# Kernel optimization log

Measured on AMD Instinct MI355X. Metric: run time of the kernel, lower is better.

Reference implementation:

```python
import jax, jax.numpy as jnp
import numpy as np

B, N, M, D = 2, 2048, 32, 128
H, DH = 8, 16
DI = H * DH            # dim_inner = 128
S = 5                  # 1 + max_degree + max_degree, max_degree = 2
DMLP = 256             # int(2.0 * dim_inner)


def _ln(x, g):  # LayerNorm(bias=False)
    mu = x.mean(-1, keepdims=True)
    var = ((x - mu) ** 2).mean(-1, keepdims=True)
    return (x - mu) / jnp.sqrt(var + 1e-5) * g


def _softclamp(t, v=50.0):
    return jnp.tanh(t / v) * v


def _gather(a, idx):  # a: [b, n, ...], idx: [b, i, j] -> [b, i, j, ...]
    return jax.vmap(lambda t, ix: jnp.take(t, ix, axis=0))(a, idx)


def setup_inputs():
    key = jax.random.key(0)
    ks = jax.random.split(key, 24)
    w = lambda k, i, o: jax.random.normal(k, (i, o), jnp.float32) / np.sqrt(i)
    return {
        'h': jax.random.normal(ks[0], (B, N, D), jnp.float32),
        't_ij': jax.random.normal(ks[1], (B, N, M, D), jnp.float32),
        'r_ij_1': jax.random.normal(ks[2], (B, N, M, 3), jnp.float32),
        'r_ij_2': jax.random.normal(ks[3], (B, N, M, 5), jnp.float32),
        'x_1': jax.random.normal(ks[4], (B, N, D, 3), jnp.float32),
        'x_2': jax.random.normal(ks[5], (B, N, D, 5), jnp.float32),
        'g_hi': jnp.ones((D,), jnp.float32),
        'g_hj': jnp.ones((D,), jnp.float32),
        'Wq': w(ks[6], D, DI),
        'Wk': w(ks[7], D, DI),
        'Wv1': w(ks[8], D, DMLP), 'bv1': jnp.zeros((DMLP,), jnp.float32),
        'Wv2': w(ks[9], DMLP, S * DI), 'bv2': jnp.zeros((S * DI,), jnp.float32),
        'Wp1': w(ks[10], D, DMLP), 'bp1': jnp.zeros((DMLP,), jnp.float32),
        'Wp2': w(ks[11], DMLP, S * DI), 'bp2': jnp.zeros((S * DI,), jnp.float32),
        'Wek': w(ks[12], D, S * DI),
        'Wev': w(ks[13], D, S * DI),
        'Wg': w(ks[14], D, H * S), 'bg': jnp.zeros((H * S,), jnp.float32),
        'Wc': w(ks[15], DI, D),
        'neighbor_indices': jax.random.randint(ks[16], (B, N, M), 0, N),
        'neighbor_mask': jnp.ones((B, N, M), bool),
    }


def reference(h, t_ij, r_ij_1, r_ij_2, x_1, x_2, g_hi, g_hj, Wq, Wk, Wv1, bv1,
              Wv2, bv2, Wp1, bp1, Wp2, bp2, Wek, Wev, Wg, bg, Wc,
              neighbor_indices, neighbor_mask):
    b, n, m = neighbor_indices.shape
    hi = _ln(h, g_hi)
    hj = _ln(h, g_hj)
    q = (hi @ Wq).reshape(b, n, H, DH).transpose(0, 2, 1, 3)               # b h i dh
    k = hj @ Wk                                                            # b n (h dh)
    v = jax.nn.silu(hj @ Wv1 + bv1) @ Wv2 + bv2                            # b n (s h dh)
    pav = jax.nn.silu(hj @ Wp1 + bp1) @ Wp2 + bp2                          # post-attn h values
    ek = jax.nn.silu(t_ij @ Wek)                                           # b i j (s h dh)
    ev = t_ij @ Wev
    # neighbor gathers over the node axis
    k_g = _gather(k, neighbor_indices)                                     # b i j (h dh)
    v_g = _gather(v, neighbor_indices)                                     # b i j (s h dh)
    pav_g = _gather(pav, neighbor_indices)
    heads4 = lambda t: t.reshape(b, n, m, H, DH).transpose(0, 3, 1, 2, 4)          # b h i j dh
    heads5 = lambda t: t.reshape(b, n, m, S, H, DH).transpose(0, 4, 1, 2, 3, 5)    # b h i j s dh
    keys = heads4(k_g)[..., None, :] * heads5(ek)                          # edge-fused keys
    sim = _softclamp(jnp.einsum('bhid,bhijsd->bhijs', q, keys))
    sim = jnp.where(neighbor_mask[:, None, :, :, None], sim, -jnp.finfo(sim.dtype).max)
    attn = jax.nn.softmax(sim, axis=-2)                                    # softmax over neighbors j
    sea = attn[..., None] * heads5(v_g) + heads5(ev) * heads5(pav_g)       # b h i j s dh
    gates = jax.nn.sigmoid(hi @ Wg + bg).reshape(b, n, H, S)               # layout (h s)
    sea = sea * gates.transpose(0, 2, 1, 3)[:, :, :, None, :, None]        # b h i 1 s 1
    out = sea.transpose(0, 2, 3, 4, 1, 5).reshape(b, n, m, S, DI) @ Wc     # b i j s d
    h_res = out[..., 0, :].sum(axis=2)                                     # sum over neighbors
    x_res = []
    for li, (r_l, x_l) in enumerate(((r_ij_1, x_1), (r_ij_2, x_2))):
        r_part = jnp.einsum('bijm,bijd->bidm', r_l, out[..., 1 + li, :])
        xg = _gather(x_l, neighbor_indices)                                # b i j d ml
        x_res.append(r_part + jnp.einsum('bijdm,bijd->bidm', xg, out[..., 3 + li, :]))
    return (h_res, x_res[0], x_res[1])
```

## Files before the change

kernel.cpp:

```cpp
#include <hip/hip_runtime.h>
#include <hip/hip_bf16.h>
#include <cstdint>


typedef __bf16 bf16x8 __attribute__((ext_vector_type(8)));
typedef float  f32x4  __attribute__((ext_vector_type(4)));
typedef unsigned short u16;
typedef unsigned int   u32;

__device__ __forceinline__ float sigm_(float x){ return 1.f/(1.f+__expf(-x)); }
__device__ __forceinline__ float silu_(float x){ return x/(1.f+__expf(-x)); }
__device__ __forceinline__ u16 f2b(float f){
    union{float f; u32 u;} x; x.f = f;
    u32 r = x.u + 0x7FFFu + ((x.u>>16)&1u);
    return (u16)(r>>16);
}
__device__ __forceinline__ float b2f(u16 b){
    union{u32 u; float f;} x; x.u = ((u32)b)<<16; return x.f;
}
union VecU { uint4 u; bf16x8 v; u16 s[8]; };
union Vec4 { uint2 u; u16 s[4]; };
__device__ __forceinline__ bf16x8 ld8(const u16* p){ VecU x; x.u = *(const uint4*)p; return x.v; }

__global__ __launch_bounds__(256) void prep_kernel(
    const float* __restrict__ Wek, const float* __restrict__ Wev,
    const float* __restrict__ Wc,
    const float* __restrict__ x1, const float* __restrict__ x2,
    u16* __restrict__ wekT, u16* __restrict__ wevT, u16* __restrict__ wcT,
    float* __restrict__ xT1, float* __restrict__ xT2, int do_xt)
{
    const int idx = blockIdx.x*256 + threadIdx.x;
    if (idx < 81920) {
        const int n = idx >> 7, k = idx & 127;
        wekT[idx] = f2b(Wek[k*640 + n]);
        wevT[idx] = f2b(Wev[k*640 + n]);
    }
    if (idx < 16384) {
        const int d = idx >> 7, c = idx & 127;
        wcT[idx] = f2b(Wc[c*128 + d]);
    }
    if (do_xt) {
        if (idx < 4096*384) {
            const int node = idx/384, rem = idx%384, m = rem>>7, d = rem&127;
            xT1[idx] = x1[((size_t)node*128 + d)*3 + m];
        }
        if (idx < 4096*640) {
            const int node = idx/640, rem = idx%640, m = rem>>7, d = rem&127;
            xT2[idx] = x2[((size_t)node*128 + d)*5 + m];
        }
    }
}

__global__ __launch_bounds__(256) void node_kernel(
    const float* __restrict__ h,
    const float* __restrict__ g_hi, const float* __restrict__ g_hj,
    const float* __restrict__ Wq, const float* __restrict__ Wk,
    const float* __restrict__ Wv1, const float* __restrict__ bv1,
    const float* __restrict__ Wv2, const float* __restrict__ bv2,
    const float* __restrict__ Wp1, const float* __restrict__ bp1,
    const float* __restrict__ Wp2, const float* __restrict__ bp2,
    const float* __restrict__ Wg, const float* __restrict__ bg,
    float* __restrict__ qws, float* __restrict__ kws,
    float* __restrict__ vws, float* __restrict__ pavws, float* __restrict__ gws)
{
    const int tid  = threadIdx.x;
    const int base = blockIdx.x * 8;
    __shared__ __align__(16) float hi_s[8][128];
    __shared__ __align__(16) float hj_s[8][128];
    __shared__ __align__(16) float u_s[8][256];

    {
        const int wv = tid >> 6, lane = tid & 63;
        for (int r = wv; r < 8; r += 4) {
            const int node = base + r;
            float a  = h[node*128 + lane];
            float b2 = h[node*128 + 64 + lane];
            float s = a + b2;
            #pragma unroll
            for (int off = 32; off > 0; off >>= 1) s += __shfl_down(s, off);
            s = __shfl(s, 0);
            const float mu = s * (1.f/128.f);
            const float da = a - mu, db = b2 - mu;
            float v = da*da + db*db;
            #pragma unroll
            for (int off = 32; off > 0; off >>= 1) v += __shfl_down(v, off);
            v = __shfl(v, 0);
            const float rstd = rsqrtf(v*(1.f/128.f) + 1e-5f);
            hi_s[r][lane]    = da*rstd*g_hi[lane];
            hi_s[r][64+lane] = db*rstd*g_hi[64+lane];
            hj_s[r][lane]    = da*rstd*g_hj[lane];
            hj_s[r][64+lane] = db*rstd*g_hj[64+lane];
        }
    }
    __syncthreads();

    {
        const int o  = tid & 127;
        const int r0 = (tid >> 7) * 4;
        float aq[4], ak[4];
        #pragma unroll
        for (int r=0;r<4;r++){ aq[r]=0.f; ak[r]=0.f; }
        for (int c0=0;c0<128;c0+=4) {
            float wq0=Wq[(c0+0)*128+o], wq1=Wq[(c0+1)*128+o], wq2=Wq[(c0+2)*128+o], wq3=Wq[(c0+3)*128+o];
            float wk0=Wk[(c0+0)*128+o], wk1=Wk[(c0+1)*128+o], wk2=Wk[(c0+2)*128+o], wk3=Wk[(c0+3)*128+o];
            #pragma unroll
            for (int r=0;r<4;r++) {
                float4 hi4 = *(const float4*)(&hi_s[r0+r][c0]);
                float4 hj4 = *(const float4*)(&hj_s[r0+r][c0]);
                aq[r] += hi4.x*wq0; aq[r] += hi4.y*wq1; aq[r] += hi4.z*wq2; aq[r] += hi4.w*wq3;
                ak[r] += hj4.x*wk0; ak[r] += hj4.y*wk1; ak[r] += hj4.z*wk2; ak[r] += hj4.w*wk3;
            }
        }
        #pragma unroll
        for (int r=0;r<4;r++) {
            qws[(size_t)(base+r0+r)*128 + o] = aq[r];
            kws[(size_t)(base+r0+r)*128 + o] = ak[r];
        }
    }

    {
        const int o = tid;
        float acc[8];
        const float bias = bv1[o];
        #pragma unroll
        for (int r=0;r<8;r++) acc[r]=bias;
        for (int c0=0;c0<128;c0+=4) {
            float w0=Wv1[(c0+0)*256+o], w1=Wv1[(c0+1)*256+o], w2=Wv1[(c0+2)*256+o], w3=Wv1[(c0+3)*256+o];
            #pragma unroll
            for (int r=0;r<8;r++) {
                float4 u4 = *(const float4*)(&hj_s[r][c0]);
                acc[r] += u4.x*w0; acc[r] += u4.y*w1; acc[r] += u4.z*w2; acc[r] += u4.w*w3;
            }
        }
        #pragma unroll
        for (int r=0;r<8;r++) u_s[r][o] = silu_(acc[r]);
    }
    __syncthreads();

    for (int o=tid; o<640; o+=256) {
        float acc[8];
        const float bias = bv2[o];
        #pragma unroll
        for (int r=0;r<8;r++) acc[r]=bias;
        for (int c0=0;c0<256;c0+=4) {
            float w0=Wv2[(c0+0)*640+o], w1=Wv2[(c0+1)*640+o], w2=Wv2[(c0+2)*640+o], w3=Wv2[(c0+3)*640+o];
            #pragma unroll
            for (int r=0;r<8;r++) {
                float4 u4 = *(const float4*)(&u_s[r][c0]);
                acc[r] += u4.x*w0; acc[r] += u4.y*w1; acc[r] += u4.z*w2; acc[r] += u4.w*w3;
            }
        }
        #pragma unroll
        for (int r=0;r<8;r++) vws[(size_t)(base+r)*640 + o] = acc[r];
    }
    __syncthreads();

    {
        const int o = tid;
        float acc[8];
        const float bias = bp1[o];
        #pragma unroll
        for (int r=0;r<8;r++) acc[r]=bias;
        for (int c0=0;c0<128;c0+=4) {
            float w0=Wp1[(c0+0)*256+o], w1=Wp1[(c0+1)*256+o], w2=Wp1[(c0+2)*256+o], w3=Wp1[(c0+3)*256+o];
            #pragma unroll
            for (int r=0;r<8;r++) {
                float4 u4 = *(const float4*)(&hj_s[r][c0]);
                acc[r] += u4.x*w0; acc[r] += u4.y*w1; acc[r] += u4.z*w2; acc[r] += u4.w*w3;
            }
        }
        #pragma unroll
        for (int r=0;r<8;r++) u_s[r][o] = silu_(acc[r]);
    }
    __syncthreads();

    for (int o=tid; o<640; o+=256) {
        float acc[8];
        const float bias = bp2[o];
        #pragma unroll
        for (int r=0;r<8;r++) acc[r]=bias;
        for (int c0=0;c0<256;c0+=4) {
            float w0=Wp2[(c0+0)*640+o], w1=Wp2[(c0+1)*640+o], w2=Wp2[(c0+2)*640+o], w3=Wp2[(c0+3)*640+o];
            #pragma unroll
            for (int r=0;r<8;r++) {
                float4 u4 = *(const float4*)(&u_s[r][c0]);
                acc[r] += u4.x*w0; acc[r] += u4.y*w1; acc[r] += u4.z*w2; acc[r] += u4.w*w3;
            }
        }
        #pragma unroll
        for (int r=0;r<8;r++) pavws[(size_t)(base+r)*640 + o] = acc[r];
    }

    for (int idx=tid; idx<8*40; idx+=256) {
        const int r = idx/40, hs = idx%40;
        float s = bg[hs];
        for (int c=0;c<128;c++) s += hi_s[r][c]*Wg[c*40+hs];
        gws[(size_t)(base+r)*40 + hs] = sigm_(s);
    }
}

template<bool XT>
__global__ __launch_bounds__(256,3) void edge_kernel(
    const float* __restrict__ t_ij,
    const float* __restrict__ r1, const float* __restrict__ r2,
    const float* __restrict__ x1, const float* __restrict__ x2,
    const float* __restrict__ xT1, const float* __restrict__ xT2,
    const u16* __restrict__ wekT, const u16* __restrict__ wevT,
    const u16* __restrict__ wcT,
    const int* __restrict__ nidx,
    const float* __restrict__ qws, const float* __restrict__ kws,
    const float* __restrict__ vws, const float* __restrict__ pavws,
    const float* __restrict__ gws,
    float* __restrict__ out)
{
    const int node = blockIdx.x;
    const int bN   = (node >> 11) << 11;
    const int tid  = threadIdx.x;
    const int lane = tid & 63, w = tid >> 6;
    const int ll   = lane & 15, lh = lane >> 4;

    __shared__ __align__(16) u16   tj_s[32*128];
    __shared__ __align__(16) u16   chunk_s[80*128];
    __shared__ float sim_s[32][40];
    __shared__ __align__(16) float q_s[128];
    __shared__ float g_s[40];
    __shared__ int   jn_s[32];

    if (tid < 32) jn_s[tid] = nidx[node*32 + tid];
    else if (tid >= 64 && tid < 192) q_s[tid-64] = qws[(size_t)node*128 + (tid-64)];
    else if (tid >= 192 && tid < 232) g_s[tid-192] = gws[(size_t)node*40 + (tid-192)];
    __syncthreads();

    bf16x8 wcf[2][4];
    #pragma unroll
    for (int dlt=0;dlt<2;dlt++)
        #pragma unroll
        for (int ks=0;ks<4;ks++)
            wcf[dlt][ks] = ld8(wcT + (size_t)((w*2+dlt)*16 + ll)*128 + ks*32 + lh*8);

    float kq[16];
    {
        const int j = tid >> 3, c0 = (tid & 7) * 16;
        const float* tp = t_ij + (size_t)node*4096 + j*128 + c0;
        float4 t0 = *(const float4*)(tp+0);
        float4 t1 = *(const float4*)(tp+4);
        float4 t2 = *(const float4*)(tp+8);
        float4 t3 = *(const float4*)(tp+12);
        VecU p0, p1;
        p0.s[0]=f2b(t0.x); p0.s[1]=f2b(t0.y); p0.s[2]=f2b(t0.z); p0.s[3]=f2b(t0.w);
        p0.s[4]=f2b(t1.x); p0.s[5]=f2b(t1.y); p0.s[6]=f2b(t1.z); p0.s[7]=f2b(t1.w);
        p1.s[0]=f2b(t2.x); p1.s[1]=f2b(t2.y); p1.s[2]=f2b(t2.z); p1.s[3]=f2b(t2.w);
        p1.s[4]=f2b(t3.x); p1.s[5]=f2b(t3.y); p1.s[6]=f2b(t3.z); p1.s[7]=f2b(t3.w);
        const int el = (j*128 + c0) ^ ((j&7)<<3);
        *(uint4*)(tj_s + el)       = p0.u;
        *(uint4*)(tj_s + (el ^ 8)) = p1.u;

        const float* kp = kws + ((size_t)(bN + jn_s[j]))*128 + c0;
        #pragma unroll
        for (int i=0;i<16;i+=4) {
            float4 kv = *(const float4*)(kp+i);
            float4 qv = *(const float4*)(&q_s[c0+i]);
            kq[i+0] = qv.x*kv.x; kq[i+1] = qv.y*kv.y;
            kq[i+2] = qv.z*kv.z; kq[i+3] = qv.w*kv.w;
        }
    }
    __syncthreads();

    for (int jh=0; jh<2; jh++) {
        bf16x8 tfr[4];
        #pragma unroll
        for (int ks=0;ks<4;ks++) {
            const int j = jh*16 + ll;
            tfr[ks] = ld8(tj_s + ((j*128 + ks*32 + lh*8) ^ ((j&7)<<3)));
        }
        #pragma unroll 2
        for (int t=0;t<10;t++) {
            const int nt = w + 4*t;
            const u16* wp = wekT + (size_t)(nt*16 + ll)*128 + lh*8;
            __builtin_amdgcn_s_setprio(1);
            f32x4 aA = {0.f,0.f,0.f,0.f}, aB = {0.f,0.f,0.f,0.f};
            aA = __builtin_amdgcn_mfma_f32_16x16x32_bf16(ld8(wp +  0), tfr[0], aA, 0,0,0);
            aB = __builtin_amdgcn_mfma_f32_16x16x32_bf16(ld8(wp + 32), tfr[1], aB, 0,0,0);
            aA = __builtin_amdgcn_mfma_f32_16x16x32_bf16(ld8(wp + 64), tfr[2], aA, 0,0,0);
            aB = __builtin_amdgcn_mfma_f32_16x16x32_bf16(ld8(wp + 96), tfr[3], aB, 0,0,0);
            __builtin_amdgcn_s_setprio(0);
            f32x4 acc = aA + aB;
            const int ss = nt >> 3, c0 = (nt&7)*16 + lh*4;
            const int r  = ss*16 + ll;
            Vec4 pk;
            #pragma unroll
            for (int reg=0;reg<4;reg++) pk.s[reg] = f2b(silu_(acc[reg]));
            *(uint2*)(chunk_s + ((r*128 + c0) ^ ((r&7)<<3))) = pk.u;
        }
        __syncthreads();

        if ((tid >> 7) == jh) {
            const int jj = (tid >> 3) & 15, hh = tid & 7;
            #pragma unroll
            for (int ss=0; ss<5; ss++) {
                const int r = ss*16 + jj;
                const int el = (r*128 + hh*16) ^ ((r&7)<<3);
                VecU e0, e1;
                e0.u = *(const uint4*)(chunk_s + el);
                e1.u = *(const uint4*)(chunk_s + (el^8));
                float s = 0.f;
                #pragma unroll
                for (int i=0;i<8;i++) s += kq[i]   * b2f(e0.s[i]);
                #pragma unroll
                for (int i=0;i<8;i++) s += kq[8+i] * b2f(e1.s[i]);
                sim_s[jh*16 + jj][hh*5 + ss] = 50.f * tanhf(s*0.02f);
            }
        }
        __syncthreads();
    }

    if (tid < 40) {
        float mx = -1e30f;
        #pragma unroll
        for (int j=0;j<32;j++) mx = fmaxf(mx, sim_s[j][tid]);
        float sum = 0.f;
        #pragma unroll
        for (int j=0;j<32;j++) sum += __expf(sim_s[j][tid]-mx);
        const float inv = 1.f/sum;
        #pragma unroll
        for (int j=0;j<32;j++) sim_s[j][tid] = __expf(sim_s[j][tid]-mx)*inv;
    }
    __syncthreads();

    float accH[2] = {0,0};
    float aR1[3][2], aX1[3][2], aR2[5][2], aX2[5][2];
    #pragma unroll
    for (int m=0;m<3;m++){ aR1[m][0]=aR1[m][1]=0.f; aX1[m][0]=aX1[m][1]=0.f; }
    #pragma unroll
    for (int m=0;m<5;m++){ aR2[m][0]=aR2[m][1]=0.f; aX2[m][0]=aX2[m][1]=0.f; }

    for (int jh=0; jh<2; jh++) {
        bf16x8 tfr[4];
        #pragma unroll
        for (int ks=0;ks<4;ks++) {
            const int j = jh*16 + ll;
            tfr[ks] = ld8(tj_s + ((j*128 + ks*32 + lh*8) ^ ((j&7)<<3)));
        }
        const int edge = jh*16 + ll;
        const int nj   = jn_s[edge];
        const float* vrow = vws   + (size_t)(bN + nj)*640;
        const float* prow = pavws + (size_t)(bN + nj)*640;

        float4 v4c = *(const float4*)(vrow + (w*16 + lh*4));
        float4 pvc = *(const float4*)(prow + (w*16 + lh*4));
        #pragma unroll 2
        for (int t=0;t<10;t++) {
            const int nt = w + 4*t;
            const float4 v4 = v4c, pv = pvc;
            if (t < 9) {
                const int o0n = (nt+4)*16 + lh*4;
                v4c = *(const float4*)(vrow + o0n);
                pvc = *(const float4*)(prow + o0n);
            }
            const u16* wp = wevT + (size_t)(nt*16 + ll)*128 + lh*8;
            __builtin_amdgcn_s_setprio(1);
            f32x4 aA = {0.f,0.f,0.f,0.f}, aB = {0.f,0.f,0.f,0.f};
            aA = __builtin_amdgcn_mfma_f32_16x16x32_bf16(ld8(wp +  0), tfr[0], aA, 0,0,0);
            aB = __builtin_amdgcn_mfma_f32_16x16x32_bf16(ld8(wp + 32), tfr[1], aB, 0,0,0);
            aA = __builtin_amdgcn_mfma_f32_16x16x32_bf16(ld8(wp + 64), tfr[2], aA, 0,0,0);
            aB = __builtin_amdgcn_mfma_f32_16x16x32_bf16(ld8(wp + 96), tfr[3], aB, 0,0,0);
            __builtin_amdgcn_s_setprio(0);
            f32x4 acc = aA + aB;
            const int ss = nt >> 3, hsu = (nt&7)*5 + ss;
            const int c0 = (nt&7)*16 + lh*4;
            const float gate = g_s[hsu];
            const float attn = sim_s[edge][hsu];
            Vec4 w4;
            w4.s[0] = f2b((attn*v4.x + acc[0]*pv.x)*gate);
            w4.s[1] = f2b((attn*v4.y + acc[1]*pv.y)*gate);
            w4.s[2] = f2b((attn*v4.z + acc[2]*pv.z)*gate);
            w4.s[3] = f2b((attn*v4.w + acc[3]*pv.w)*gate);
            const int r = ss*16 + ll;
            *(uint2*)(chunk_s + ((r*128 + c0) ^ ((r&7)<<3))) = w4.u;
        }
        __syncthreads();

        #pragma unroll 1
        for (int mt=0; mt<5; ++mt) {
            bf16x8 afr[4];
            #pragma unroll
            for (int ks=0;ks<4;ks++) {
                const int r = mt*16 + ll;
                afr[ks] = ld8(chunk_s + ((r*128 + ks*32 + lh*8) ^ ((r&7)<<3)));
            }
            #pragma unroll
            for (int dlt=0; dlt<2; ++dlt) {
                __builtin_amdgcn_s_setprio(1);
                f32x4 dA = {0.f,0.f,0.f,0.f}, dB = {0.f,0.f,0.f,0.f};
                dA = __builtin_amdgcn_mfma_f32_16x16x32_bf16(afr[0], wcf[dlt][0], dA, 0,0,0);
                dB = __builtin_amdgcn_mfma_f32_16x16x32_bf16(afr[1], wcf[dlt][1], dB, 0,0,0);
                dA = __builtin_amdgcn_mfma_f32_16x16x32_bf16(afr[2], wcf[dlt][2], dA, 0,0,0);
                dB = __builtin_amdgcn_mfma_f32_16x16x32_bf16(afr[3], wcf[dlt][3], dB, 0,0,0);
                __builtin_amdgcn_s_setprio(0);
                f32x4 dacc = dA + dB;
                const int d = (w*2+dlt)*16 + ll;
                if (mt == 0) {
                    accH[dlt] += dacc[0]+dacc[1]+dacc[2]+dacc[3];
                } else if (mt == 1) {
                    #pragma unroll
                    for (int reg=0;reg<4;reg++) {
                        const int j = jh*16 + lh*4 + reg;
                        const float* rp = r1 + ((size_t)node*32 + j)*3;
                        const float p = dacc[reg];
                        #pragma unroll
                        for (int m=0;m<3;m++) aR1[m][dlt] += rp[m]*p;
                    }
                } else if (mt == 2) {
                    #pragma unroll
                    for (int reg=0;reg<4;reg++) {
                        const int j = jh*16 + lh*4 + reg;
                        const float* rp = r2 + ((size_t)node*32 + j)*5;
                        const float p = dacc[reg];
                        #pragma unroll
                        for (int m=0;m<5;m++) aR2[m][dlt] += rp[m]*p;
                    }
                } else if (mt == 3) {
                    #pragma unroll
                    for (int reg=0;reg<4;reg++) {
                        const int j = jh*16 + lh*4 + reg;
                        const int njg = jn_s[j];
                        const float p = dacc[reg];
                        if (XT) {
                            const float* xp = xT1 + ((size_t)(bN + njg)*3)*128 + d;
                            #pragma unroll
                            for (int m=0;m<3;m++) aX1[m][dlt] += xp[m*128]*p;
                        } else {
                            const float* xp = x1 + ((size_t)(bN + njg)*128 + d)*3;
                            #pragma unroll
                            for (int m=0;m<3;m++) aX1[m][dlt] += xp[m]*p;
                        }
                    }
                } else {
                    #pragma unroll
                    for (int reg=0;reg<4;reg++) {
                        const int j = jh*16 + lh*4 + reg;
                        const int njg = jn_s[j];
                        const float p = dacc[reg];
                        if (XT) {
                            const float* xp = xT2 + ((size_t)(bN + njg)*5)*128 + d;
                            #pragma unroll
                            for (int m=0;m<5;m++) aX2[m][dlt] += xp[m*128]*p;
                        } else {
                            const float* xp = x2 + ((size_t)(bN + njg)*128 + d)*5;
                            #pragma unroll
                            for (int m=0;m<5;m++) aX2[m][dlt] += xp[m]*p;
                        }
                    }
                }
            }
        }
        __syncthreads();
    }

    #define RED2(x) { x += __shfl_xor(x,16); x += __shfl_xor(x,32); }
    #pragma unroll
    for (int dlt=0; dlt<2; ++dlt) {
        RED2(accH[dlt]);
        #pragma unroll
        for (int m=0;m<3;m++){ RED2(aR1[m][dlt]); RED2(aX1[m][dlt]); }
        #pragma unroll
        for (int m=0;m<5;m++){ RED2(aR2[m][dlt]); RED2(aX2[m][dlt]); }
    }
    if (lh == 0) {
        #pragma unroll
        for (int dlt=0; dlt<2; ++dlt) {
            const int d = (w*2+dlt)*16 + ll;
            out[(size_t)node*128 + d] = accH[dlt];
            float* o1 = out + 524288 + ((size_t)node*128 + d)*3;
            #pragma unroll
            for (int m=0;m<3;m++) o1[m] = aR1[m][dlt] + aX1[m][dlt];
            float* o2 = out + 2097152 + ((size_t)node*128 + d)*5;
            #pragma unroll
            for (int m=0;m<5;m++) o2[m] = aR2[m][dlt] + aX2[m][dlt];
        }
    }
}

extern "C" void kernel_launch(void* const* d_in, const int* in_sizes, int n_in,
                              void* d_out, int out_size, void* d_ws, size_t ws_size,
                              hipStream_t stream)
{
    const float* h    = (const float*)d_in[0];
    const float* t_ij = (const float*)d_in[1];
    const float* r1   = (const float*)d_in[2];
    const float* r2   = (const float*)d_in[3];
    const float* x1   = (const float*)d_in[4];
    const float* x2   = (const float*)d_in[5];
    const float* g_hi = (const float*)d_in[6];
    const float* g_hj = (const float*)d_in[7];
    const float* Wq   = (const float*)d_in[8];
    const float* Wk   = (const float*)d_in[9];
    const float* Wv1  = (const float*)d_in[10];
    const float* bv1  = (const float*)d_in[11];
    const float* Wv2  = (const float*)d_in[12];
    const float* bv2  = (const float*)d_in[13];
    const float* Wp1  = (const float*)d_in[14];
    const float* bp1  = (const float*)d_in[15];
    const float* Wp2  = (const float*)d_in[16];
    const float* bp2  = (const float*)d_in[17];
    const float* Wek  = (const float*)d_in[18];
    const float* Wev  = (const float*)d_in[19];
    const float* Wg   = (const float*)d_in[20];
    const float* bg   = (const float*)d_in[21];
    const float* Wc   = (const float*)d_in[22];
    const int*   nidx = (const int*)d_in[23];

    char* ws = (char*)d_ws;
    float* qws   = (float*)ws;  ws += (size_t)4096*128*4;
    float* kws   = (float*)ws;  ws += (size_t)4096*128*4;
    float* gws   = (float*)ws;  ws += (size_t)4096*40*4;
    float* vws   = (float*)ws;  ws += (size_t)4096*640*4;
    float* pavws = (float*)ws;  ws += (size_t)4096*640*4;
    u16*   wekT  = (u16*)ws;    ws += (size_t)81920*2;
    u16*   wevT  = (u16*)ws;    ws += (size_t)81920*2;
    u16*   wcT   = (u16*)ws;    ws += (size_t)16384*2;
    float* xT1   = (float*)ws;  ws += (size_t)4096*384*4;
    float* xT2   = (float*)ws;  ws += (size_t)4096*640*4;
    const size_t need_xt = (size_t)(ws - (char*)d_ws);
    const int use_xt = (ws_size >= need_xt) ? 1 : 0;

    hipLaunchKernelGGL(prep_kernel, dim3(use_xt ? 10240 : 320), dim3(256), 0, stream,
        Wek, Wev, Wc, x1, x2, wekT, wevT, wcT, xT1, xT2, use_xt);

    hipLaunchKernelGGL(node_kernel, dim3(512), dim3(256), 0, stream,
        h, g_hi, g_hj, Wq, Wk, Wv1, bv1, Wv2, bv2, Wp1, bp1, Wp2, bp2, Wg, bg,
        qws, kws, vws, pavws, gws);

    if (use_xt) {
        hipLaunchKernelGGL(edge_kernel<true>, dim3(4096), dim3(256), 0, stream,
            t_ij, r1, r2, x1, x2, xT1, xT2, wekT, wevT, wcT, nidx,
            qws, kws, vws, pavws, gws, (float*)d_out);
    } else {
        hipLaunchKernelGGL(edge_kernel<false>, dim3(4096), dim3(256), 0, stream,
            t_ij, r1, r2, x1, x2, xT1, xT2, wekT, wevT, wcT, nidx,
            qws, kws, vws, pavws, gws, (float*)d_out);
    }
}
```

Before: 577.3 us.

## Split edge kernel into two 256-thread groups processing neighbor halves concurrently

The edge kernel goes from 256 to 512 threads per block. Each group of 256 threads handles one half of the 32 neighbors in parallel, where before a single group looped over the halves one after another. Each group gets its own chunk buffer in shared memory, and the groups' partial reductions are combined through shared memory before the final write. This removes the serial loop over halves and several block barriers, but it doubles chunk shared memory, keeps the Wc fragments in registers in both groups, and adds a cross-group reduction step. The launch bounds change to (512,4), which may limit registers per thread.

```diff
diff --git a/kernel.cpp b/kernel.cpp
--- a/kernel.cpp
+++ b/kernel.cpp
@@ -200,7 +200,7 @@
 }
 
 template<bool XT>
-__global__ __launch_bounds__(256,3) void edge_kernel(
+__global__ __launch_bounds__(512,4) void edge_kernel(
     const float* __restrict__ t_ij,
     const float* __restrict__ r1, const float* __restrict__ r2,
     const float* __restrict__ x1, const float* __restrict__ x2,
@@ -216,16 +216,20 @@
     const int node = blockIdx.x;
     const int bN   = (node >> 11) << 11;
     const int tid  = threadIdx.x;
-    const int lane = tid & 63, w = tid >> 6;
+    const int grp  = tid >> 8;
+    const int ltid = tid & 255;
+    const int lane = ltid & 63, w = ltid >> 6;
     const int ll   = lane & 15, lh = lane >> 4;
 
     __shared__ __align__(16) u16   tj_s[32*128];
-    __shared__ __align__(16) u16   chunk_s[80*128];
+    __shared__ __align__(16) u16   chunk_s[2][80*128];
     __shared__ float sim_s[32][40];
     __shared__ __align__(16) float q_s[128];
     __shared__ float g_s[40];
     __shared__ int   jn_s[32];
 
+    u16* chunk = chunk_s[grp];
+
     if (tid < 32) jn_s[tid] = nidx[node*32 + tid];
     else if (tid >= 64 && tid < 192) q_s[tid-64] = qws[(size_t)node*128 + (tid-64)];
     else if (tid >= 192 && tid < 232) g_s[tid-192] = gws[(size_t)node*40 + (tid-192)];
@@ -239,8 +243,8 @@
             wcf[dlt][ks] = ld8(wcT + (size_t)((w*2+dlt)*16 + ll)*128 + ks*32 + lh*8);
 
     float kq[16];
-    {
-        const int j = tid >> 3, c0 = (tid & 7) * 16;
+    if (ltid < 128) {
+        const int j = grp*16 + (ltid >> 3), c0 = (ltid & 7) * 16;
         const float* tp = t_ij + (size_t)node*4096 + j*128 + c0;
         float4 t0 = *(const float4*)(tp+0);
         float4 t1 = *(const float4*)(tp+4);
@@ -266,53 +270,51 @@
     }
     __syncthreads();
 
-    for (int jh=0; jh<2; jh++) {
-        bf16x8 tfr[4];
-        #pragma unroll
-        for (int ks=0;ks<4;ks++) {
-            const int j = jh*16 + ll;
-            tfr[ks] = ld8(tj_s + ((j*128 + ks*32 + lh*8) ^ ((j&7)<<3)));
-        }
-        #pragma unroll 2
-        for (int t=0;t<10;t++) {
-            const int nt = w + 4*t;
-            const u16* wp = wekT + (size_t)(nt*16 + ll)*128 + lh*8;
-            __builtin_amdgcn_s_setprio(1);
-            f32x4 aA = {0.f,0.f,0.f,0.f}, aB = {0.f,0.f,0.f,0.f};
-            aA = __builtin_amdgcn_mfma_f32_16x16x32_bf16(ld8(wp +  0), tfr[0], aA, 0,0,0);
-            aB = __builtin_amdgcn_mfma_f32_16x16x32_bf16(ld8(wp + 32), tfr[1], aB, 0,0,0);
-            aA = __builtin_amdgcn_mfma_f32_16x16x32_bf16(ld8(wp + 64), tfr[2], aA, 0,0,0);
-            aB = __builtin_amdgcn_mfma_f32_16x16x32_bf16(ld8(wp + 96), tfr[3], aB, 0,0,0);
-            __builtin_amdgcn_s_setprio(0);
-            f32x4 acc = aA + aB;
-            const int ss = nt >> 3, c0 = (nt&7)*16 + lh*4;
-            const int r  = ss*16 + ll;
-            Vec4 pk;
-            #pragma unroll
-            for (int reg=0;reg<4;reg++) pk.s[reg] = f2b(silu_(acc[reg]));
-            *(uint2*)(chunk_s + ((r*128 + c0) ^ ((r&7)<<3))) = pk.u;
-        }
-        __syncthreads();
-
-        if ((tid >> 7) == jh) {
-            const int jj = (tid >> 3) & 15, hh = tid & 7;
-            #pragma unroll
-            for (int ss=0; ss<5; ss++) {
-                const int r = ss*16 + jj;
-                const int el = (r*128 + hh*16) ^ ((r&7)<<3);
-                VecU e0, e1;
-                e0.u = *(const uint4*)(chunk_s + el);
-                e1.u = *(const uint4*)(chunk_s + (el^8));
-                float s = 0.f;
-                #pragma unroll
-                for (int i=0;i<8;i++) s += kq[i]   * b2f(e0.s[i]);
-                #pragma unroll
-                for (int i=0;i<8;i++) s += kq[8+i] * b2f(e1.s[i]);
-                sim_s[jh*16 + jj][hh*5 + ss] = 50.f * tanhf(s*0.02f);
-            }
-        }
-        __syncthreads();
-    }
+    bf16x8 tfr[4];
+    #pragma unroll
+    for (int ks=0;ks<4;ks++) {
+        const int j = grp*16 + ll;
+        tfr[ks] = ld8(tj_s + ((j*128 + ks*32 + lh*8) ^ ((j&7)<<3)));
+    }
+    #pragma unroll 2
+    for (int t=0;t<10;t++) {
+        const int nt = w + 4*t;
+        const u16* wp = wekT + (size_t)(nt*16 + ll)*128 + lh*8;
+        __builtin_amdgcn_s_setprio(1);
+        f32x4 aA = {0.f,0.f,0.f,0.f}, aB = {0.f,0.f,0.f,0.f};
+        aA = __builtin_amdgcn_mfma_f32_16x16x32_bf16(ld8(wp +  0), tfr[0], aA, 0,0,0);
+        aB = __builtin_amdgcn_mfma_f32_16x16x32_bf16(ld8(wp + 32), tfr[1], aB, 0,0,0);
+        aA = __builtin_amdgcn_mfma_f32_16x16x32_bf16(ld8(wp + 64), tfr[2], aA, 0,0,0);
+        aB = __builtin_amdgcn_mfma_f32_16x16x32_bf16(ld8(wp + 96), tfr[3], aB, 0,0,0);
+        __builtin_amdgcn_s_setprio(0);
+        f32x4 acc = aA + aB;
+        const int ss = nt >> 3, c0 = (nt&7)*16 + lh*4;
+        const int r  = ss*16 + ll;
+        Vec4 pk;
+        #pragma unroll
+        for (int reg=0;reg<4;reg++) pk.s[reg] = f2b(silu_(acc[reg]));
+        *(uint2*)(chunk + ((r*128 + c0) ^ ((r&7)<<3))) = pk.u;
+    }
+    __syncthreads();
+
+    if (ltid < 128) {
+        const int jj = ltid >> 3, hh = ltid & 7;
+        #pragma unroll
+        for (int ss=0; ss<5; ss++) {
+            const int r = ss*16 + jj;
+            const int el = (r*128 + hh*16) ^ ((r&7)<<3);
+            VecU e0, e1;
+            e0.u = *(const uint4*)(chunk + el);
+            e1.u = *(const uint4*)(chunk + (el^8));
+            float s = 0.f;
+            #pragma unroll
+            for (int i=0;i<8;i++) s += kq[i]   * b2f(e0.s[i]);
+            #pragma unroll
+            for (int i=0;i<8;i++) s += kq[8+i] * b2f(e1.s[i]);
+            sim_s[grp*16 + jj][hh*5 + ss] = 50.f * tanhf(s*0.02f);
+        }
+    }
+    __syncthreads();
 
     if (tid < 40) {
         float mx = -1e30f;
@@ -334,14 +336,8 @@
     #pragma unroll
     for (int m=0;m<5;m++){ aR2[m][0]=aR2[m][1]=0.f; aX2[m][0]=aX2[m][1]=0.f; }
 
-    for (int jh=0; jh<2; jh++) {
-        bf16x8 tfr[4];
-        #pragma unroll
-        for (int ks=0;ks<4;ks++) {
-            const int j = jh*16 + ll;
-            tfr[ks] = ld8(tj_s + ((j*128 + ks*32 + lh*8) ^ ((j&7)<<3)));
-        }
-        const int edge = jh*16 + ll;
+    {
+        const int edge = grp*16 + ll;
         const int nj   = jn_s[edge];
         const float* vrow = vws   + (size_t)(bN + nj)*640;
         const float* prow = pavws + (size_t)(bN + nj)*640;
@@ -376,85 +372,84 @@
             w4.s[2] = f2b((attn*v4.z + acc[2]*pv.z)*gate);
             w4.s[3] = f2b((attn*v4.w + acc[3]*pv.w)*gate);
             const int r = ss*16 + ll;
-            *(uint2*)(chunk_s + ((r*128 + c0) ^ ((r&7)<<3))) = w4.u;
-        }
-        __syncthreads();
-
-        #pragma unroll 1
-        for (int mt=0; mt<5; ++mt) {
-            bf16x8 afr[4];
-            #pragma unroll
-            for (int ks=0;ks<4;ks++) {
-                const int r = mt*16 + ll;
-                afr[ks] = ld8(chunk_s + ((r*128 + ks*32 + lh*8) ^ ((r&7)<<3)));
-            }
-            #pragma unroll
-            for (int dlt=0; dlt<2; ++dlt) {
-                __builtin_amdgcn_s_setprio(1);
-                f32x4 dA = {0.f,0.f,0.f,0.f}, dB = {0.f,0.f,0.f,0.f};
-                dA = __builtin_amdgcn_mfma_f32_16x16x32_bf16(afr[0], wcf[dlt][0], dA, 0,0,0);
-                dB = __builtin_amdgcn_mfma_f32_16x16x32_bf16(afr[1], wcf[dlt][1], dB, 0,0,0);
-                dA = __builtin_amdgcn_mfma_f32_16x16x32_bf16(afr[2], wcf[dlt][2], dA, 0,0,0);
-                dB = __builtin_amdgcn_mfma_f32_16x16x32_bf16(afr[3], wcf[dlt][3], dB, 0,0,0);
-                __builtin_amdgcn_s_setprio(0);
-                f32x4 dacc = dA + dB;
-                const int d = (w*2+dlt)*16 + ll;
-                if (mt == 0) {
-                    accH[dlt] += dacc[0]+dacc[1]+dacc[2]+dacc[3];
-                } else if (mt == 1) {
+            *(uint2*)(chunk + ((r*128 + c0) ^ ((r&7)<<3))) = w4.u;
+        }
+    }
+    __syncthreads();
+
+    #pragma unroll 1
+    for (int mt=0; mt<5; ++mt) {
+        bf16x8 afr[4];
+        #pragma unroll
+        for (int ks=0;ks<4;ks++) {
+            const int r = mt*16 + ll;
+            afr[ks] = ld8(chunk + ((r*128 + ks*32 + lh*8) ^ ((r&7)<<3)));
+        }
+        #pragma unroll
+        for (int dlt=0; dlt<2; ++dlt) {
+            __builtin_amdgcn_s_setprio(1);
+            f32x4 dA = {0.f,0.f,0.f,0.f}, dB = {0.f,0.f,0.f,0.f};
+            dA = __builtin_amdgcn_mfma_f32_16x16x32_bf16(afr[0], wcf[dlt][0], dA, 0,0,0);
+            dB = __builtin_amdgcn_mfma_f32_16x16x32_bf16(afr[1], wcf[dlt][1], dB, 0,0,0);
+            dA = __builtin_amdgcn_mfma_f32_16x16x32_bf16(afr[2], wcf[dlt][2], dA, 0,0,0);
+            dB = __builtin_amdgcn_mfma_f32_16x16x32_bf16(afr[3], wcf[dlt][3], dB, 0,0,0);
+            __builtin_amdgcn_s_setprio(0);
+            f32x4 dacc = dA + dB;
+            const int d = (w*2+dlt)*16 + ll;
+            if (mt == 0) {
+                accH[dlt] += dacc[0]+dacc[1]+dacc[2]+dacc[3];
+            } else if (mt == 1) {
+                #pragma unroll
+                for (int reg=0;reg<4;reg++) {
+                    const int j = grp*16 + lh*4 + reg;
+                    const float* rp = r1 + ((size_t)node*32 + j)*3;
+                    const float p = dacc[reg];
                     #pragma unroll
-                    for (int reg=0;reg<4;reg++) {
-                        const int j = jh*16 + lh*4 + reg;
-                        const float* rp = r1 + ((size_t)node*32 + j)*3;
-                        const float p = dacc[reg];
+                    for (int m=0;m<3;m++) aR1[m][dlt] += rp[m]*p;
+                }
+            } else if (mt == 2) {
+                #pragma unroll
+                for (int reg=0;reg<4;reg++) {
+                    const int j = grp*16 + lh*4 + reg;
+                    const float* rp = r2 + ((size_t)node*32 + j)*5;
+                    const float p = dacc[reg];
+                    #pragma unroll
+                    for (int m=0;m<5;m++) aR2[m][dlt] += rp[m]*p;
+                }
+            } else if (mt == 3) {
+                #pragma unroll
+                for (int reg=0;reg<4;reg++) {
+                    const int j = grp*16 + lh*4 + reg;
+                    const int njg = jn_s[j];
+                    const float p = dacc[reg];
+                    if (XT) {
+                        const float* xp = xT1 + ((size_t)(bN + njg)*3)*128 + d;
                         #pragma unroll
-                        for (int m=0;m<3;m++) aR1[m][dlt] += rp[m]*p;
-                    }
-                } else if (mt == 2) {
-                    #pragma unroll
-                    for (int reg=0;reg<4;reg++) {
-                        const int j = jh*16 + lh*4 + reg;
-                        const float* rp = r2 + ((size_t)node*32 + j)*5;
-                        const float p = dacc[reg];
+                        for (int m=0;m<3;m++) aX1[m][dlt] += xp[m*128]*p;
+                    } else {
+                        const float* xp = x1 + ((size_t)(bN + njg)*128 + d)*3;
                         #pragma unroll
-                        for (int m=0;m<5;m++) aR2[m][dlt] += rp[m]*p;
-                    }
-                } else if (mt == 3) {
-                    #pragma unroll
-                    for (int reg=0;reg<4;reg++) {
-                        const int j = jh*16 + lh*4 + reg;
-                        const int njg = jn_s[j];
-                        const float p = dacc[reg];
-                        if (XT) {
-                            const float* xp = xT1 + ((size_t)(bN + njg)*3)*128 + d;
-                            #pragma unroll
-                            for (int m=0;m<3;m++) aX1[m][dlt] += xp[m*128]*p;
-                        } else {
-                            const float* xp = x1 + ((size_t)(bN + njg)*128 + d)*3;
-                            #pragma unroll
-                            for (int m=0;m<3;m++) aX1[m][dlt] += xp[m]*p;
-                        }
-                    }
-                } else {
-                    #pragma unroll
-                    for (int reg=0;reg<4;reg++) {
-                        const int j = jh*16 + lh*4 + reg;
-                        const int njg = jn_s[j];
-                        const float p = dacc[reg];
-                        if (XT) {
-                            const float* xp = xT2 + ((size_t)(bN + njg)*5)*128 + d;
-                            #pragma unroll
-                            for (int m=0;m<5;m++) aX2[m][dlt] += xp[m*128]*p;
-                        } else {
-                            const float* xp = x2 + ((size_t)(bN + njg)*128 + d)*5;
-                            #pragma unroll
-                            for (int m=0;m<5;m++) aX2[m][dlt] += xp[m]*p;
-                        }
+                        for (int m=0;m<3;m++) aX1[m][dlt] += xp[m]*p;
                     }
                 }
-            }
-        }
-        __syncthreads();
+            } else {
+                #pragma unroll
+                for (int reg=0;reg<4;reg++) {
+                    const int j = grp*16 + lh*4 + reg;
+                    const int njg = jn_s[j];
+                    const float p = dacc[reg];
+                    if (XT) {
+                        const float* xp = xT2 + ((size_t)(bN + njg)*5)*128 + d;
+                        #pragma unroll
+                        for (int m=0;m<5;m++) aX2[m][dlt] += xp[m*128]*p;
+                    } else {
+                        const float* xp = x2 + ((size_t)(bN + njg)*128 + d)*5;
+                        #pragma unroll
+                        for (int m=0;m<5;m++) aX2[m][dlt] += xp[m]*p;
+                    }
+                }
+            }
+        }
     }
 
     #define RED2(x) { x += __shfl_xor(x,16); x += __shfl_xor(x,32); }
@@ -466,17 +461,34 @@
         #pragma unroll
         for (int m=0;m<5;m++){ RED2(aR2[m][dlt]); RED2(aX2[m][dlt]); }
     }
-    if (lh == 0) {
+    __syncthreads();
+
+    float* xch = (float*)chunk_s[0];
+    if (grp == 1 && lh == 0) {
         #pragma unroll
         for (int dlt=0; dlt<2; ++dlt) {
             const int d = (w*2+dlt)*16 + ll;
-            out[(size_t)node*128 + d] = accH[dlt];
+            float* p = xch + d*17;
+            p[0] = accH[dlt];
+            #pragma unroll
+            for (int m=0;m<3;m++){ p[1+m] = aR1[m][dlt]; p[4+m] = aX1[m][dlt]; }
+            #pragma unroll
+            for (int m=0;m<5;m++){ p[7+m] = aR2[m][dlt]; p[12+m] = aX2[m][dlt]; }
+        }
+    }
+    __syncthreads();
+    if (grp == 0 && lh == 0) {
+        #pragma unroll
+        for (int dlt=0; dlt<2; ++dlt) {
+            const int d = (w*2+dlt)*16 + ll;
+            const float* p = xch + d*17;
+            out[(size_t)node*128 + d] = accH[dlt] + p[0];
             float* o1 = out + 524288 + ((size_t)node*128 + d)*3;
             #pragma unroll
-            for (int m=0;m<3;m++) o1[m] = aR1[m][dlt] + aX1[m][dlt];
+            for (int m=0;m<3;m++) o1[m] = (aR1[m][dlt] + p[1+m]) + (aX1[m][dlt] + p[4+m]);
             float* o2 = out + 2097152 + ((size_t)node*128 + d)*5;
             #pragma unroll
-            for (int m=0;m<5;m++) o2[m] = aR2[m][dlt] + aX2[m][dlt];
+            for (int m=0;m<5;m++) o2[m] = (aR2[m][dlt] + p[7+m]) + (aX2[m][dlt] + p[12+m]);
         }
     }
 }
@@ -532,11 +544,11 @@
         qws, kws, vws, pavws, gws);
 
     if (use_xt) {
-        hipLaunchKernelGGL(edge_kernel<true>, dim3(4096), dim3(256), 0, stream,
+        hipLaunchKernelGGL(edge_kernel<true>, dim3(4096), dim3(512), 0, stream,
             t_ij, r1, r2, x1, x2, xT1, xT2, wekT, wevT, wcT, nidx,
             qws, kws, vws, pavws, gws, (float*)d_out);
     } else {
-        hipLaunchKernelGGL(edge_kernel<false>, dim3(4096), dim3(256), 0, stream,
+        hipLaunchKernelGGL(edge_kernel<false>, dim3(4096), dim3(512), 0, stream,
             t_ij, r1, r2, x1, x2, xT1, xT2, wekT, wevT, wcT, nidx,
             qws, kws, vws, pavws, gws, (float*)d_out);
     }
```

New measurement: 596.6 us. 3.3% more time.
